# Performance work log

Hardware: AMD Instinct MI355X
Metric: run time of the kernel (lower is better)

The kernel has to match this reference:

```python
import jax, jax.numpy as jnp
import numpy as np

NEG = -1e30  # log-space 'zero' (avoids -inf NaN issues under jit)
EPS = 1e-7   # keras.backend.epsilon()


def _ctc_loss(y_true, y_pred):
    # y_true: [B, L] int labels in [0, C-1), y_pred: [B, T, C] softmax probs.
    # Keras ctc_batch_cost: logits = log(y_pred + eps), then tf.nn.ctc_loss
    # (which applies log_softmax internally), blank = C - 1.
    B, T, C = y_pred.shape
    L = y_true.shape[1]
    S = 2 * L + 1
    blank = C - 1

    logp = jax.nn.log_softmax(jnp.log(y_pred + EPS), axis=-1)  # [B, T, C]

    # Extended label sequence: blank, l1, blank, l2, ..., blank  -> [B, S]
    ext = jnp.full((B, S), blank, dtype=y_true.dtype).at[:, 1::2].set(y_true)
    lp_ext = jnp.take_along_axis(logp, ext[:, None, :].astype(jnp.int32), axis=2)  # [B, T, S]

    # skip transition s-2 -> s allowed iff ext[s] != blank and ext[s] != ext[s-2]
    ext_m2 = jnp.concatenate([jnp.full((B, 2), blank, ext.dtype), ext[:, :-2]], axis=1)
    allow_skip = (ext != blank) & (ext != ext_m2)
    allow_skip = allow_skip.at[:, :2].set(False)

    # alpha init at t=0
    alpha = jnp.full((B, S), NEG, dtype=logp.dtype)
    alpha = alpha.at[:, 0].set(lp_ext[:, 0, 0]).at[:, 1].set(lp_ext[:, 0, 1])

    neg1 = jnp.full((B, 1), NEG, dtype=logp.dtype)
    neg2 = jnp.full((B, 2), NEG, dtype=logp.dtype)

    def step(a, lp_t):
        prev1 = jnp.concatenate([neg1, a[:, :-1]], axis=1)
        prev2 = jnp.concatenate([neg2, a[:, :-2]], axis=1)
        acc = jnp.logaddexp(a, prev1)
        acc = jnp.where(allow_skip, jnp.logaddexp(acc, prev2), acc)
        return acc + lp_t, None

    lp_seq = jnp.transpose(lp_ext, (1, 0, 2))[1:]  # [T-1, B, S]
    alpha, _ = jax.lax.scan(step, alpha, lp_seq)

    loss = -jnp.logaddexp(alpha[:, -1], alpha[:, -2])  # [B]
    return loss[:, None]  # [B, 1] like keras ctc_batch_cost


def setup_inputs() -> dict:
    key = jax.random.key(0)
    k1, k2 = jax.random.split(key)
    B, T, C, L = 1024, 256, 128, 64
    y_true = jax.random.randint(k1, (B, L), 0, C - 1, dtype=jnp.int32)
    y_pred = jax.random.uniform(k2, (B, T, C), dtype=jnp.float32, minval=1e-4, maxval=1.0)
    return {"y_true": y_true, "y_pred": y_pred}


def reference(y_true, y_pred):
    return _ctc_loss(y_true, y_pred)
```

## Files before the change

### kernel.cpp

```cpp
#include <hip/hip_runtime.h>
#include <math.h>

#define BATCH 1024
#define TT    256
#define CC    128
#define LL    64
#define EPSV  (1e-7f)

typedef float f32x4 __attribute__((ext_vector_type(4)));
typedef __fp16 fp16x2 __attribute__((ext_vector_type(2)));

template <int CTRL>
__device__ __forceinline__ float dpp0(float x) {
    return __int_as_float(__builtin_amdgcn_update_dpp(0, __float_as_int(x), CTRL, 0xF, 0xF, true));
}
template <int CTRL>
__device__ __forceinline__ float dppS(float x) {
    return __int_as_float(__builtin_amdgcn_update_dpp(__float_as_int(x), __float_as_int(x), CTRL, 0xF, 0xF, false));
}
__device__ __forceinline__ float rol1_f(float x) {
    return __int_as_float(__builtin_amdgcn_update_dpp(__float_as_int(x), __float_as_int(x), 0x134, 0xF, 0xF, false));
}
__device__ __forceinline__ int rol1_i(int x) {
    return __builtin_amdgcn_update_dpp(x, x, 0x134, 0xF, 0xF, false);
}
__device__ __forceinline__ float rdlane(float x, int l) {
    return __int_as_float(__builtin_amdgcn_readlane(__float_as_int(x), l));
}
__device__ __forceinline__ float wave_max_bcast(float m) {
    m = fmaxf(m, dppS<0x111>(m));
    m = fmaxf(m, dppS<0x112>(m));
    m = fmaxf(m, dppS<0x114>(m));
    m = fmaxf(m, dppS<0x118>(m));
    m = fmaxf(m, dppS<0x142>(m));
    m = fmaxf(m, dppS<0x143>(m));
    return rdlane(m, 63);
}
__device__ __forceinline__ int pkrtz(float a, float b) {
    fp16x2 h = __builtin_amdgcn_cvt_pkrtz(a, b);
    int r; __builtin_memcpy(&r, &h, 4);
    return r;
}
__device__ __forceinline__ float h2f(unsigned short u) {
    _Float16 h; __builtin_memcpy(&h, &u, 2);
    return (float)h;
}

__global__ __launch_bounds__(512, 8) void ctc_fwd_kernel(const int* __restrict__ y_true,
                                                         const float* __restrict__ y_pred,
                                                         float* __restrict__ out) {
    __shared__ unsigned qtab32[128][64];
    __shared__ float qblank[TT];
    __shared__ float logZpart[8];
    __shared__ int   chunkCnt[32];
    __shared__ int   doneCnt;

    const int b    = blockIdx.x;
    const int tid  = threadIdx.x;
    const int wv   = tid >> 6;
    const int lane = tid & 63;

    const float* yp = y_pred + (size_t)b * (TT * CC);
    const int lab  = y_true[b * LL + lane];
    const int srcA = lab >> 2;
    const int srcB = 32 + srcA;
    const bool hiPair = (lab & 2) != 0;
    const bool hiHalf = (lab & 1) != 0;

    const int off = ((lane >> 5) << 7) + ((lane & 31) << 2);
    const float* base = yp + off;

    if (tid < 32) chunkCnt[tid] = 0;
    if (tid == 32) doneCnt = 0;
    __syncthreads();

    if (wv > 0) {
        const int sw = wv - 1;
        float prodM = 1.0f;
        int   expS  = 0;
        f32x4 v[8];
        #pragma unroll
        for (int d = 0; d < 8; ++d) {
            int r2 = sw + 7 * d; r2 = (r2 < 128) ? r2 : 127;
            v[d] = *(const f32x4*)(base + 256 * r2);
        }
        #pragma unroll
        for (int i = 0; i < 19; ++i) {
            const int  r2i   = sw + 7 * i;
            const bool valid = (r2i < 128);
            const int  r2    = valid ? r2i : 127;
            f32x4 x = v[i & 7];
            if (i + 8 < 19) {
                int rn = sw + 7 * (i + 8); rn = (rn < 128) ? rn : 127;
                v[i & 7] = *(const f32x4*)(base + 256 * rn);
            }
            float q0 = x[0] + EPSV, q1 = x[1] + EPSV;
            float q2 = x[2] + EPSV, q3 = x[3] + EPSV;
            float s = (q0 + q1) + (q2 + q3);
            s += dpp0<0x111>(s);
            s += dpp0<0x112>(s);
            s += dpp0<0x114>(s);
            s += dpp0<0x118>(s);
            s += dpp0<0x142>(s);
            unsigned bits = __float_as_uint(s);
            if (valid) {
                expS += (int)((bits >> 23) & 0xFF) - 127;
                prodM *= __uint_as_float((bits & 0x007FFFFFu) | 0x3F800000u);
            }
            int i01 = pkrtz(q0, q1);
            int i23 = pkrtz(q2, q3);
            int X = (lane < 32) ? i01 : i23;
            int Y = (lane < 32) ? i23 : i01;
            int u = __shfl(X, hiPair ? srcB : srcA);
            int w = __shfl(Y, hiPair ? srcA : srcB);
            int sA = hiPair ? w : u;
            int sB = hiPair ? u : w;
            unsigned hA = hiHalf ? ((unsigned)sA >> 16) : ((unsigned)sA & 0xFFFF);
            unsigned hB = hiHalf ? ((unsigned)sB >> 16) : ((unsigned)sB & 0xFFFF);
            if (valid) {
                qtab32[r2][lane] = hA | (hB << 16);
                if ((lane & 31) == 31) qblank[2 * r2 + (lane >> 5)] = q3;
                asm volatile("s_waitcnt lgkmcnt(0)" ::: "memory");
                if (lane == 0) atomicAdd(&chunkCnt[r2 >> 2], 1);
            }
        }
        float zlog = __logf(prodM) + (float)expS * 0.69314718055994531f;
        float z31 = rdlane(zlog, 31), z63 = rdlane(zlog, 63);
        if (lane == 0) {
            logZpart[wv] = z31 + z63;
            asm volatile("s_waitcnt lgkmcnt(0)" ::: "memory");
            atomicAdd(&doneCnt, 1);
        }
    } else {
        const int   labm1 = rol1_i(lab);
        const float mskip = (lane >= 1 && lab != labm1) ? 1.0f : 0.0f;
        const bool  l0 = (lane == 0);

        volatile int* vcnt = chunkCnt;
        while (vcnt[0] < 4) __builtin_amdgcn_s_sleep(1);
        __builtin_amdgcn_sched_barrier(0);

        float a0 = l0 ? qblank[0] : 0.0f;
        float a1 = l0 ? h2f((unsigned short)(qtab32[0][lane] & 0xFFFF)) : 0.0f;
        float aX = 0.0f;
        int Esum = 0;

        {
            unsigned q4[4];
            #pragma unroll
            for (int j = 0; j < 4; ++j) q4[j] = qtab32[j][lane];
            float qb8[8], ql8[8];
            #pragma unroll
            for (int i = 1; i < 8; ++i) {
                qb8[i] = qblank[i];
                unsigned uu = q4[i >> 1];
                ql8[i] = h2f((unsigned short)((i & 1) ? (uu >> 16) : (uu & 0xFFFF)));
            }
            #pragma unroll
            for (int i = 1; i < 8; ++i) {
                float nb  = rol1_f(a1);
                float na0 = (a0 + (l0 ? 0.0f : nb)) * qb8[i];
                float na1 = fmaf(mskip, nb, a0 + a1) * ql8[i];
                aX = l0 ? (aX + nb) * qb8[i] : 0.0f;
                a0 = na0; a1 = na1;
            }
            float mall = wave_max_bcast(fmaxf(fmaxf(a0, a1), aX));
            int e = 127 - (int)((__float_as_uint(mall) >> 23) & 0xFF);
            float sc = __uint_as_float((unsigned)(127 + e) << 23);
            a0 *= sc; a1 *= sc; aX *= sc;
            Esum += e;
        }
        for (int c = 1; c < 32; ++c) {
            while (vcnt[c] < 4) __builtin_amdgcn_s_sleep(1);
            __builtin_amdgcn_sched_barrier(0);
            unsigned q4[4];
            #pragma unroll
            for (int j = 0; j < 4; ++j) q4[j] = qtab32[4 * c + j][lane];
            float qb8[8], ql8[8];
            #pragma unroll
            for (int i = 0; i < 8; ++i) {
                qb8[i] = qblank[8 * c + i];
                unsigned uu = q4[i >> 1];
                ql8[i] = h2f((unsigned short)((i & 1) ? (uu >> 16) : (uu & 0xFFFF)));
            }
            #pragma unroll
            for (int i = 0; i < 8; ++i) {
                float nb  = rol1_f(a1);
                float na0 = (a0 + (l0 ? 0.0f : nb)) * qb8[i];
                float na1 = fmaf(mskip, nb, a0 + a1) * ql8[i];
                aX = l0 ? (aX + nb) * qb8[i] : 0.0f;
                a0 = na0; a1 = na1;
            }
            float mall = wave_max_bcast(fmaxf(fmaxf(a0, a1), aX));
            int e = 127 - (int)((__float_as_uint(mall) >> 23) & 0xFF);
            float sc = __uint_as_float((unsigned)(127 + e) << 23);
            a0 *= sc; a1 *= sc; aX *= sc;
            Esum += e;
        }
        volatile int* vd = &doneCnt;
        while (*vd < 7) __builtin_amdgcn_s_sleep(1);
        __builtin_amdgcn_sched_barrier(0);
        float LZ = 0.0f;
        #pragma unroll
        for (int w = 1; w < 8; ++w) LZ += logZpart[w];
        float a127 = rdlane(a1, 63);
        if (lane == 0) {
            out[b] = LZ + (float)Esum * 0.69314718055994531f - __logf(aX + a127);
        }
    }
}

extern "C" void kernel_launch(void* const* d_in, const int* in_sizes, int n_in,
                              void* d_out, int out_size, void* d_ws, size_t ws_size,
                              hipStream_t stream) {
    const int*   y_true = (const int*)d_in[0];
    const float* y_pred = (const float*)d_in[1];
    float*       out    = (float*)d_out;
    ctc_fwd_kernel<<<BATCH, 512, 0, stream>>>(y_true, y_pred, out);
}
```

Before: 36.50 us.

## Assign contiguous pair ranges to producer waves and batch chunk-count atomics

Producer waves now each stream a contiguous block of 18 (or 20 for the last) row pairs instead of taking every seventh pair. This removes the clamp and valid predicates from the unrolled loop. The shared-memory counter atomic and its waitcnt now fire once per two pairs with an increment of 2, instead of once per pair. The risk is that the serial consumer wave now waits for one producer to finish several pairs before chunk 0 is ready, which delays the start of the recursion and changes how production overlaps with consumption.

```diff
diff --git a/kernel.cpp b/kernel.cpp
--- a/kernel.cpp
+++ b/kernel.cpp
@@ -46,6 +46,58 @@
     return (float)h;
 }
 
+struct StreamCtx {
+    const float* base;
+    unsigned (*qtab32)[64];
+    float* qblank;
+    int* chunkCnt;
+    int lane, srcA, srcB;
+    bool hiPair, hiHalf;
+};
+
+template <int NP>
+__device__ __forceinline__ void stream_range(const StreamCtx& c, int startPair,
+                                             float& prodM, int& expS) {
+    f32x4 v[8];
+    #pragma unroll
+    for (int d = 0; d < 8; ++d)
+        v[d] = *(const f32x4*)(c.base + 256 * (startPair + d));
+    #pragma unroll
+    for (int i = 0; i < NP; ++i) {
+        const int r2 = startPair + i;
+        f32x4 x = v[i & 7];
+        if (i + 8 < NP)
+            v[i & 7] = *(const f32x4*)(c.base + 256 * (r2 + 8));
+        float q0 = x[0] + EPSV, q1 = x[1] + EPSV;
+        float q2 = x[2] + EPSV, q3 = x[3] + EPSV;
+        float s = (q0 + q1) + (q2 + q3);
+        s += dpp0<0x111>(s);
+        s += dpp0<0x112>(s);
+        s += dpp0<0x114>(s);
+        s += dpp0<0x118>(s);
+        s += dpp0<0x142>(s);
+        unsigned bits = __float_as_uint(s);
+        expS += (int)((bits >> 23) & 0xFF) - 127;
+        prodM *= __uint_as_float((bits & 0x007FFFFFu) | 0x3F800000u);
+        int i01 = pkrtz(q0, q1);
+        int i23 = pkrtz(q2, q3);
+        int X = (c.lane < 32) ? i01 : i23;
+        int Y = (c.lane < 32) ? i23 : i01;
+        int u = __shfl(X, c.hiPair ? c.srcB : c.srcA);
+        int w = __shfl(Y, c.hiPair ? c.srcA : c.srcB);
+        int sA = c.hiPair ? w : u;
+        int sB = c.hiPair ? u : w;
+        unsigned hA = c.hiHalf ? ((unsigned)sA >> 16) : ((unsigned)sA & 0xFFFF);
+        unsigned hB = c.hiHalf ? ((unsigned)sB >> 16) : ((unsigned)sB & 0xFFFF);
+        c.qtab32[r2][c.lane] = hA | (hB << 16);
+        if ((c.lane & 31) == 31) c.qblank[2 * r2 + (c.lane >> 5)] = q3;
+        if (i & 1) {
+            asm volatile("s_waitcnt lgkmcnt(0)" ::: "memory");
+            if (c.lane == 0) atomicAdd(&c.chunkCnt[r2 >> 2], 2);
+        }
+    }
+}
+
 __global__ __launch_bounds__(512, 8) void ctc_fwd_kernel(const int* __restrict__ y_true,
                                                          const float* __restrict__ y_pred,
                                                          float* __restrict__ out) {
@@ -75,55 +127,12 @@
     __syncthreads();
 
     if (wv > 0) {
-        const int sw = wv - 1;
+        StreamCtx c{base, qtab32, qblank, chunkCnt, lane, srcA, srcB, hiPair, hiHalf};
         float prodM = 1.0f;
         int   expS  = 0;
-        f32x4 v[8];
-        #pragma unroll
-        for (int d = 0; d < 8; ++d) {
-            int r2 = sw + 7 * d; r2 = (r2 < 128) ? r2 : 127;
-            v[d] = *(const f32x4*)(base + 256 * r2);
-        }
-        #pragma unroll
-        for (int i = 0; i < 19; ++i) {
-            const int  r2i   = sw + 7 * i;
-            const bool valid = (r2i < 128);
-            const int  r2    = valid ? r2i : 127;
-            f32x4 x = v[i & 7];
-            if (i + 8 < 19) {
-                int rn = sw + 7 * (i + 8); rn = (rn < 128) ? rn : 127;
-                v[i & 7] = *(const f32x4*)(base + 256 * rn);
-            }
-            float q0 = x[0] + EPSV, q1 = x[1] + EPSV;
-            float q2 = x[2] + EPSV, q3 = x[3] + EPSV;
-            float s = (q0 + q1) + (q2 + q3);
-            s += dpp0<0x111>(s);
-            s += dpp0<0x112>(s);
-            s += dpp0<0x114>(s);
-            s += dpp0<0x118>(s);
-            s += dpp0<0x142>(s);
-            unsigned bits = __float_as_uint(s);
-            if (valid) {
-                expS += (int)((bits >> 23) & 0xFF) - 127;
-                prodM *= __uint_as_float((bits & 0x007FFFFFu) | 0x3F800000u);
-            }
-            int i01 = pkrtz(q0, q1);
-            int i23 = pkrtz(q2, q3);
-            int X = (lane < 32) ? i01 : i23;
-            int Y = (lane < 32) ? i23 : i01;
-            int u = __shfl(X, hiPair ? srcB : srcA);
-            int w = __shfl(Y, hiPair ? srcA : srcB);
-            int sA = hiPair ? w : u;
-            int sB = hiPair ? u : w;
-            unsigned hA = hiHalf ? ((unsigned)sA >> 16) : ((unsigned)sA & 0xFFFF);
-            unsigned hB = hiHalf ? ((unsigned)sB >> 16) : ((unsigned)sB & 0xFFFF);
-            if (valid) {
-                qtab32[r2][lane] = hA | (hB << 16);
-                if ((lane & 31) == 31) qblank[2 * r2 + (lane >> 5)] = q3;
-                asm volatile("s_waitcnt lgkmcnt(0)" ::: "memory");
-                if (lane == 0) atomicAdd(&chunkCnt[r2 >> 2], 1);
-            }
-        }
+        const int startPair = 18 * (wv - 1);
+        if (wv < 7) stream_range<18>(c, startPair, prodM, expS);
+        else        stream_range<20>(c, startPair, prodM, expS);
         float zlog = __logf(prodM) + (float)expS * 0.69314718055994531f;
         float z31 = rdlane(zlog, 31), z63 = rdlane(zlog, 63);
         if (lane == 0) {
@@ -170,16 +179,16 @@
             a0 *= sc; a1 *= sc; aX *= sc;
             Esum += e;
         }
-        for (int c = 1; c < 32; ++c) {
-            while (vcnt[c] < 4) __builtin_amdgcn_s_sleep(1);
+        for (int cIdx = 1; cIdx < 32; ++cIdx) {
+            while (vcnt[cIdx] < 4) __builtin_amdgcn_s_sleep(1);
             __builtin_amdgcn_sched_barrier(0);
             unsigned q4[4];
             #pragma unroll
-            for (int j = 0; j < 4; ++j) q4[j] = qtab32[4 * c + j][lane];
+            for (int j = 0; j < 4; ++j) q4[j] = qtab32[4 * cIdx + j][lane];
             float qb8[8], ql8[8];
             #pragma unroll
             for (int i = 0; i < 8; ++i) {
-                qb8[i] = qblank[8 * c + i];
+                qb8[i] = qblank[8 * cIdx + i];
                 unsigned uu = q4[i >> 1];
                 ql8[i] = h2f((unsigned short)((i & 1) ? (uu >> 16) : (uu & 0xFFFF)));
             }
```

Result: slower. 47.35 us (+29.8%).
